# Optimization experiments

Measured on AMD Instinct MI355X. Metric: run time of the kernel, lower is better.

The kernel has to match this reference:

```python
import jax, jax.numpy as jnp
import numpy as np

OUT_CHN, IN_CHN, K = 256, 256, 3
STRIDE, PADDING = 1, 1

def binary_activation(x):
    # STE: forward = sign(x), backward = piecewise-polynomial surrogate out3
    m1 = (x < -1).astype(x.dtype)
    m2 = (x < 0).astype(x.dtype)
    m3 = (x < 1).astype(x.dtype)
    out1 = -1.0 * m1 + (x * x + 2 * x) * (1 - m1)
    out2 = out1 * m2 + (-x * x + 2 * x) * (1 - m2)
    out3 = out2 * m3 + 1.0 * (1 - m3)
    return jax.lax.stop_gradient(jnp.sign(x)) - jax.lax.stop_gradient(out3) + out3

def setup_inputs() -> dict:
    key = jax.random.key(0)
    kx, kw = jax.random.split(key)
    x = jax.random.normal(kx, (32, IN_CHN, 56, 56), dtype=jnp.float32)
    # weights stored flat [N,1] as in the torch module, scaled by 0.001
    weights = jax.random.uniform(kw, (OUT_CHN * IN_CHN * K * K, 1), dtype=jnp.float32) * 0.001
    return {"x": x, "weights": weights}

def reference(x, weights):
    w = weights.reshape(OUT_CHN, IN_CHN, K, K)
    # STE for weights: forward = sign(w), backward = clamp(w,-1,1)
    clipped = jnp.clip(w, -1.0, 1.0)
    bw = jax.lax.stop_gradient(jnp.sign(w)) - jax.lax.stop_gradient(clipped) + clipped
    bx = binary_activation(x)
    y = jax.lax.conv_general_dilated(
        bx, bw,
        window_strides=(STRIDE, STRIDE),
        padding=[(PADDING, PADDING), (PADDING, PADDING)],
        dimension_numbers=("NCHW", "OIHW", "NCHW"),
    )
    return y
```

## Files before the change

kernel.cpp:

```cpp
#include <hip/hip_runtime.h>
#include <stdint.h>

#define N_BATCH 32
#define CHN     256
#define HW      56
#define HP      58

#define XPAD_CELLS (N_BATCH * HP * 2 * HP)
#define XPAD_U32   (XPAD_CELLS * 4)

__global__ __launch_bounds__(256) void prep_kernel(const float* __restrict__ x,
                                                   const float* __restrict__ wsrc,
                                                   uint32_t* __restrict__ xpad,
                                                   uint32_t* __restrict__ wbits,
                                                   int* __restrict__ wpop) {
    __shared__ int part[9][4];
    int bid  = blockIdx.x;
    int t    = threadIdx.x;
    int lane = t & 63;

    if (bid < 784) {
        int tid = bid * 256 + t;
        int n   = tid / 6272;
        int rem = tid - n * 6272;
        int hf  = rem / 3136;
        int pq  = rem - hf * 3136;

        const float* src = x + ((size_t)(n * 256 + hf * 128)) * 3136 + pq;
        uint32_t b0 = 0, b1 = 0, b2 = 0, b3 = 0;
#pragma unroll
        for (int g = 0; g < 8; g++) {
            float v[16];
#pragma unroll
            for (int i = 0; i < 16; i++) v[i] = src[(size_t)(g * 16 + i) * 3136];
#pragma unroll
            for (int i = 0; i < 16; i++) {
                int c = g * 16 + i;
                uint32_t b = v[i] > 0.0f ? 1u : 0u;
                if ((c >> 5) == 0) b0 |= b << (c & 31);
                else if ((c >> 5) == 1) b1 |= b << (c & 31);
                else if ((c >> 5) == 2) b2 |= b << (c & 31);
                else b3 |= b << (c & 31);
            }
        }
        int h = pq / 56;
        int w = pq - h * 56;
        uint32_t cell = ((uint32_t)(n * HP + h + 1) * 2 + hf) * HP + (w + 1);
        ((uint4*)xpad)[cell] = make_uint4(b0, b1, b2, b3);
    } else if (bid < 841) {
        int u = (bid - 784) * 256 + t;
        if (u < 14592) {
            int p = u / 228;
            int e = u - p * 228;
            int n = p >> 1, h = p & 1;
            int hp, wp;
            if (e < 58)       { hp = 0;       wp = e;       }
            else if (e < 116) { hp = 57;      wp = e - 58;  }
            else if (e < 172) { hp = e - 115; wp = 0;       }
            else              { hp = e - 171; wp = 57;      }
            uint32_t cell = ((uint32_t)(n * HP + hp) * 2 + h) * HP + wp;
            ((uint4*)xpad)[cell] = make_uint4(0u, 0u, 0u, 0u);
        }
    } else {
        int o  = bid - 841;
        int wv = t >> 6;
        const float* p = wsrc + ((size_t)o * 256 + t) * 9;
        float v[9];
#pragma unroll
        for (int tap = 0; tap < 9; tap++) v[tap] = p[tap];
#pragma unroll
        for (int tap = 0; tap < 9; tap++) {
            unsigned long long m = __ballot(v[tap] > 0.0f);
            if (lane == 0) {
                wbits[(size_t)(o * 9 + tap) * 8 + 2 * wv]     = (uint32_t)m;
                wbits[(size_t)(o * 9 + tap) * 8 + 2 * wv + 1] = (uint32_t)(m >> 32);
                part[tap][wv] = __builtin_popcountll(m);
            }
        }
        __syncthreads();
        if (t < 9) wpop[o * 9 + t] = part[t][0] + part[t][1] + part[t][2] + part[t][3];
    }
}

__global__ __launch_bounds__(256, 2)
void conv_kernel(const uint32_t* __restrict__ xpad,
                 const uint32_t* __restrict__ wbits,
                 const int* __restrict__ wpop,
                 float* __restrict__ out) {
    __shared__ uint4 sx[3 * 2 * HP];
    __shared__ float obuf[4 * 64 * 57];

    int t    = threadIdx.x;
    int lane = t & 63;
    int wv   = t >> 6;
    int h    = blockIdx.x;
    int n    = blockIdx.y;

    const uint4* xg = (const uint4*)xpad + ((size_t)n * HP + h) * (2 * HP);
    for (int i = t; i < 3 * 2 * HP; i += 256) sx[i] = xg[i];

    int o = wv * 64 + lane;
    const uint4* wsrc4 = (const uint4*)(wbits + (size_t)o * 72);
    uint4 W4[18];
#pragma unroll
    for (int i = 0; i < 18; i++) W4[i] = wsrc4[i];

    const int* wpa = wpop + (size_t)o * 9;
    int pa[9];
#pragma unroll
    for (int i = 0; i < 9; i++) pa[i] = wpa[i];

    __syncthreads();

    float* ob = obuf + wv * (64 * 57);
    bool hedge = (h == 0) | (h == 55);

#pragma unroll 2
    for (int w = 0; w < 56; w++) {
        const uint4* cb = sx + w;
        int a0 = 0, a1 = 0, a2 = 0, a3 = 0;
#pragma unroll
        for (int r = 0; r < 3; r++)
#pragma unroll
            for (int dw = 0; dw < 3; dw++)
#pragma unroll
                for (int hf = 0; hf < 2; hf++) {
                    uint4 Xc = cb[(r * 2 + hf) * HP + dw];
                    uint4 Wc = W4[(r * 3 + dw) * 2 + hf];
                    a0 += __builtin_popcount(Xc.x ^ Wc.x);
                    a1 += __builtin_popcount(Xc.y ^ Wc.y);
                    a2 += __builtin_popcount(Xc.z ^ Wc.z);
                    a3 += __builtin_popcount(Xc.w ^ Wc.w);
                }
        int va = 2304 - 2 * ((a0 + a1) + (a2 + a3));
        if (hedge | (w == 0) | (w == 55)) {
            int ca = 0;
#pragma unroll
            for (int dh = 0; dh < 3; dh++)
#pragma unroll
                for (int dw = 0; dw < 3; dw++)
                    if ((unsigned)(h + dh - 1) >= 56u || (unsigned)(w + dw - 1) >= 56u)
                        ca += 256 - 2 * pa[dh * 3 + dw];
            va -= ca;
        }
        ob[lane * 57 + w] = (float)va;
    }

    __syncthreads();

    if (lane < 56) {
        float* orow = out + (((size_t)n * 256 + wv * 64) * 56 + h) * 56 + lane;
#pragma unroll 8
        for (int o2 = 0; o2 < 64; o2++)
            orow[(size_t)o2 * 3136] = ob[o2 * 57 + lane];
    }
}

extern "C" void kernel_launch(void* const* d_in, const int* in_sizes, int n_in,
                              void* d_out, int out_size, void* d_ws, size_t ws_size,
                              hipStream_t stream) {
    const float* x    = (const float*)d_in[0];
    const float* wsrc = (const float*)d_in[1];
    float* out = (float*)d_out;

    uint32_t* xpad  = (uint32_t*)d_ws;
    uint32_t* wbits = xpad + XPAD_U32;
    int*      wpop  = (int*)(wbits + 256 * 9 * 8);

    prep_kernel<<<1097, 256, 0, stream>>>(x, wsrc, xpad, wbits, wpop);
    conv_kernel<<<dim3(HW, N_BATCH), 256, 0, stream>>>(xpad, wbits, wpop, out);
}
```

Baseline: 299.9 us.

## Slide register window over input columns, shrink output staging to short, raise occupancy

The conv loop now keeps three input columns (6 uint4 each) in registers and rotates them. Each new output pixel therefore loads only one new column from shared memory instead of re-reading all 18 cells. The output staging buffer changes from float to short, halving its LDS footprint, and launch bounds ask for 4 blocks per CU. The __syncthreads before write-out is dropped because each wave only reads its own staging region. Holding the weights and three columns in registers adds VGPR pressure, which under the tighter launch bound may cause spills.

```diff
diff --git a/kernel.cpp b/kernel.cpp
--- a/kernel.cpp
+++ b/kernel.cpp
@@ -82,13 +82,13 @@
     }
 }
 
-__global__ __launch_bounds__(256, 2)
+__global__ __launch_bounds__(256, 4)
 void conv_kernel(const uint32_t* __restrict__ xpad,
                  const uint32_t* __restrict__ wbits,
                  const int* __restrict__ wpop,
                  float* __restrict__ out) {
     __shared__ uint4 sx[3 * 2 * HP];
-    __shared__ float obuf[4 * 64 * 57];
+    __shared__ short obuf[4 * 64 * 57];
 
     int t    = threadIdx.x;
     int lane = t & 63;
@@ -112,47 +112,79 @@
 
     __syncthreads();
 
-    float* ob = obuf + wv * (64 * 57);
+    short* ob  = obuf + wv * (64 * 57) + lane * 57;
     bool hedge = (h == 0) | (h == 55);
 
-#pragma unroll 2
-    for (int w = 0; w < 56; w++) {
-        const uint4* cb = sx + w;
-        int a0 = 0, a1 = 0, a2 = 0, a3 = 0;
-#pragma unroll
-        for (int r = 0; r < 3; r++)
-#pragma unroll
-            for (int dw = 0; dw < 3; dw++)
-#pragma unroll
-                for (int hf = 0; hf < 2; hf++) {
-                    uint4 Xc = cb[(r * 2 + hf) * HP + dw];
-                    uint4 Wc = W4[(r * 3 + dw) * 2 + hf];
-                    a0 += __builtin_popcount(Xc.x ^ Wc.x);
-                    a1 += __builtin_popcount(Xc.y ^ Wc.y);
-                    a2 += __builtin_popcount(Xc.z ^ Wc.z);
-                    a3 += __builtin_popcount(Xc.w ^ Wc.w);
-                }
-        int va = 2304 - 2 * ((a0 + a1) + (a2 + a3));
-        if (hedge | (w == 0) | (w == 55)) {
-            int ca = 0;
-#pragma unroll
-            for (int dh = 0; dh < 3; dh++)
-#pragma unroll
-                for (int dw = 0; dw < 3; dw++)
-                    if ((unsigned)(h + dh - 1) >= 56u || (unsigned)(w + dw - 1) >= 56u)
-                        ca += 256 - 2 * pa[dh * 3 + dw];
-            va -= ca;
-        }
-        ob[lane * 57 + w] = (float)va;
+#define LOADCOL(X, c)                                                          \
+    do {                                                                       \
+        _Pragma("unroll")                                                      \
+        for (int rr = 0; rr < 6; rr++) X[rr] = sx[rr * HP + (c)];              \
+    } while (0)
+
+#define COMPUTE(P, Q, R, wpx)                                                  \
+    do {                                                                       \
+        int a0 = 0, a1 = 0, a2 = 0, a3 = 0;                                    \
+        _Pragma("unroll")                                                      \
+        for (int r = 0; r < 3; r++) {                                          \
+            _Pragma("unroll")                                                  \
+            for (int hf = 0; hf < 2; hf++) {                                   \
+                uint4 xa = P[r * 2 + hf], wa = W4[(r * 3 + 0) * 2 + hf];       \
+                a0 += __builtin_popcount(xa.x ^ wa.x);                         \
+                a1 += __builtin_popcount(xa.y ^ wa.y);                         \
+                a2 += __builtin_popcount(xa.z ^ wa.z);                         \
+                a3 += __builtin_popcount(xa.w ^ wa.w);                         \
+                uint4 xb = Q[r * 2 + hf], wb = W4[(r * 3 + 1) * 2 + hf];       \
+                a0 += __builtin_popcount(xb.x ^ wb.x);                         \
+                a1 += __builtin_popcount(xb.y ^ wb.y);                         \
+                a2 += __builtin_popcount(xb.z ^ wb.z);                         \
+                a3 += __builtin_popcount(xb.w ^ wb.w);                         \
+                uint4 xc = R[r * 2 + hf], wc = W4[(r * 3 + 2) * 2 + hf];       \
+                a0 += __builtin_popcount(xc.x ^ wc.x);                         \
+                a1 += __builtin_popcount(xc.y ^ wc.y);                         \
+                a2 += __builtin_popcount(xc.z ^ wc.z);                         \
+                a3 += __builtin_popcount(xc.w ^ wc.w);                         \
+            }                                                                  \
+        }                                                                      \
+        int va = 2304 - 2 * ((a0 + a1) + (a2 + a3));                           \
+        int wq = (wpx);                                                        \
+        if (hedge | (wq == 0) | (wq == 55)) {                                  \
+            int ca = 0;                                                        \
+            _Pragma("unroll")                                                  \
+            for (int dh = 0; dh < 3; dh++)                                     \
+                _Pragma("unroll")                                              \
+                for (int dw = 0; dw < 3; dw++)                                 \
+                    if ((unsigned)(h + dh - 1) >= 56u ||                       \
+                        (unsigned)(wq + dw - 1) >= 56u)                        \
+                        ca += 256 - 2 * pa[dh * 3 + dw];                       \
+            va -= ca;                                                          \
+        }                                                                      \
+        ob[wq] = (short)va;                                                    \
+    } while (0)
+
+    uint4 XA[6], XB[6], XC[6];
+    LOADCOL(XA, 0);
+    LOADCOL(XB, 1);
+
+    int w = 0;
+#pragma unroll 1
+    for (int i = 0; i < 18; i++) {
+        LOADCOL(XC, w + 2); COMPUTE(XA, XB, XC, w);
+        LOADCOL(XA, w + 3); COMPUTE(XB, XC, XA, w + 1);
+        LOADCOL(XB, w + 4); COMPUTE(XC, XA, XB, w + 2);
+        w += 3;
     }
-
-    __syncthreads();
+    LOADCOL(XC, 56); COMPUTE(XA, XB, XC, 54);
+    LOADCOL(XA, 57); COMPUTE(XB, XC, XA, 55);
+
+#undef LOADCOL
+#undef COMPUTE
 
     if (lane < 56) {
+        const short* obw = obuf + wv * (64 * 57);
         float* orow = out + (((size_t)n * 256 + wv * 64) * 56 + h) * 56 + lane;
 #pragma unroll 8
         for (int o2 = 0; o2 < 64; o2++)
-            orow[(size_t)o2 * 3136] = ob[o2 * 57 + lane];
+            orow[(size_t)o2 * 3136] = (float)obw[o2 * 57 + lane];
     }
 }
 
```

Result: slower. 531.4 us (+77.2%).
